# Performance work log

Measured on AMD Instinct MI355X. Metric: run time of the kernel, lower is better.

## Reference

```python
import jax, jax.numpy as jnp
import numpy as np


def _gcn(A, x, W, b):
    # GCNConv(improved=True): add_remaining_self_loops(fill=2), symmetric normalization.
    n = A.shape[0]
    idx = jnp.arange(n)
    d = jnp.diagonal(A)
    Ahat = A.at[idx, idx].set(jnp.where(d == 0, 2.0, d))  # keep existing self-loop weights
    dinv = 1.0 / jnp.sqrt(Ahat.sum(axis=1))
    return (Ahat * dinv[:, None] * dinv[None, :]) @ (x @ W) + b


def _augment(A):
    # GraphUNet.augment_adj: add self loops, A @ A (spspmm), remove self loops.
    n = A.shape[0]
    idx = jnp.arange(n)
    A1 = A.at[idx, idx].add(1.0)
    return (A1 @ A1).at[idx, idx].set(0.0)


def _pool(A, x, p, k):
    # TopKPooling with tanh nonlinearity.
    score = jnp.tanh((x @ p) / jnp.linalg.norm(p))
    vals, perm = jax.lax.top_k(score, k)
    return A[perm][:, perm], x[perm] * vals[:, None], perm


def _gat(mask, x, W, a_src, a_dst, b, heads, c, concat):
    # GATConv, eval mode (attention dropout inactive). mask[dst, src] includes self loops.
    n = x.shape[0]
    h = (x @ W).reshape(n, heads, c)
    es = jnp.einsum('shc,hc->sh', h, a_src)
    ed = jnp.einsum('dhc,hc->dh', h, a_dst)
    logits = jax.nn.leaky_relu(ed[:, None, :] + es[None, :, :], 0.2)  # [dst, src, h]
    logits = jnp.where(mask[:, :, None], logits, jnp.finfo(logits.dtype).min)
    alpha = jax.nn.softmax(logits, axis=1)  # softmax over sources per destination
    out = jnp.einsum('dsh,shc->dhc', alpha, h)
    out = out.reshape(n, heads * c) if concat else out.mean(axis=1)
    return out + b


def setup_inputs() -> dict:
    key = jax.random.key(0)
    ks = jax.random.split(key, 34)
    N, E, IN, H, OUT, HEADS = 4096, 65536, 3, 64, 128, 4
    r = lambda k, s: jax.random.normal(k, s, jnp.float32) * 0.1
    inp = {}
    inp['x'] = jax.random.normal(ks[0], (N, IN), jnp.float32)
    inp['edge_index'] = jax.random.randint(ks[1], (2, E), 0, N)
    inp['unet_w0'] = r(ks[2], (IN, H)); inp['unet_b0'] = jnp.zeros((H,), jnp.float32)
    inp['unet_w1'] = r(ks[3], (H, H)); inp['unet_b1'] = jnp.zeros((H,), jnp.float32)
    inp['unet_w2'] = r(ks[4], (H, H)); inp['unet_b2'] = jnp.zeros((H,), jnp.float32)
    inp['unet_w3'] = r(ks[5], (H, H)); inp['unet_b3'] = jnp.zeros((H,), jnp.float32)
    inp['pool_p1'] = r(ks[6], (H,)); inp['pool_p2'] = r(ks[7], (H,)); inp['pool_p3'] = r(ks[8], (H,))
    inp['up_w0'] = r(ks[9], (H, H)); inp['up_b0'] = jnp.zeros((H,), jnp.float32)
    inp['up_w1'] = r(ks[10], (H, H)); inp['up_b1'] = jnp.zeros((H,), jnp.float32)
    inp['up_w2'] = r(ks[11], (H, OUT)); inp['up_b2'] = jnp.zeros((OUT,), jnp.float32)
    inp['ln_g'] = jnp.ones((OUT,), jnp.float32); inp['ln_b'] = jnp.zeros((OUT,), jnp.float32)
    inp['res_w'] = r(ks[12], (OUT, OUT)); inp['res_b'] = jnp.zeros((OUT,), jnp.float32)
    inp['gat1_w'] = r(ks[13], (OUT, HEADS * OUT))
    inp['gat1_asrc'] = r(ks[14], (HEADS, OUT)); inp['gat1_adst'] = r(ks[15], (HEADS, OUT))
    inp['gat1_b'] = jnp.zeros((HEADS * OUT,), jnp.float32)
    inp['gat2_w'] = r(ks[16], (HEADS * OUT, OUT))
    inp['gat2_asrc'] = r(ks[17], (1, OUT)); inp['gat2_adst'] = r(ks[18], (1, OUT))
    inp['gat2_b'] = jnp.zeros((OUT,), jnp.float32)
    return inp


def reference(x, edge_index, unet_w0, unet_b0, unet_w1, unet_b1, unet_w2, unet_b2,
              unet_w3, unet_b3, pool_p1, pool_p2, pool_p3, up_w0, up_b0, up_w1, up_b1,
              up_w2, up_b2, ln_g, ln_b, res_w, res_b, gat1_w, gat1_asrc, gat1_adst,
              gat1_b, gat2_w, gat2_asrc, gat2_adst, gat2_b):
    n0 = x.shape[0]
    # Dense weighted adjacency A[dst, src]; duplicate edges accumulate weight (scatter-add).
    A0 = jnp.zeros((n0, n0), x.dtype).at[edge_index[1], edge_index[0]].add(1.0)
    # ---- GraphUNet down path ----
    x0 = jax.nn.relu(_gcn(A0, x, unet_w0, unet_b0))
    k1 = (n0 + 1) // 2
    A1, h1, perm1 = _pool(_augment(A0), x0, pool_p1, k1)
    x1 = jax.nn.relu(_gcn(A1, h1, unet_w1, unet_b1))
    k2 = (k1 + 1) // 2
    A2, h2, perm2 = _pool(_augment(A1), x1, pool_p2, k2)
    x2 = jax.nn.relu(_gcn(A2, h2, unet_w2, unet_b2))
    k3 = (k2 + 1) // 2
    A3, h3, perm3 = _pool(_augment(A2), x2, pool_p3, k3)
    x3 = jax.nn.relu(_gcn(A3, h3, unet_w3, unet_b3))
    # ---- up path (sum_res=True) ----
    h = x2 + jnp.zeros_like(x2).at[perm3].set(x3)
    h = jax.nn.relu(_gcn(A2, h, up_w0, up_b0))
    h = x1 + jnp.zeros_like(x1).at[perm2].set(h)
    h = jax.nn.relu(_gcn(A1, h, up_w1, up_b1))
    h = x0 + jnp.zeros_like(x0).at[perm1].set(h)
    h = _gcn(A0, h, up_w2, up_b2)  # last up conv: no activation -> [n0, 128]
    # ---- LayerNorm(eps=1e-6) ----
    mu = h.mean(-1, keepdims=True)
    var = ((h - mu) ** 2).mean(-1, keepdims=True)
    u = (h - mu) / jnp.sqrt(var + 1e-6) * ln_g + ln_b
    residual = u @ res_w + res_b
    mask = (A0 > 0) | jnp.eye(n0, dtype=bool)  # GATConv adds self loops
    g = jax.nn.elu(_gat(mask, u, gat1_w, gat1_asrc, gat1_adst, gat1_b, 4, 128, True))
    g = _gat(mask, g, gat2_w, gat2_asrc, gat2_adst, gat2_b, 1, 128, False)
    return g + residual
```

## Files before the change

### kernel.cpp

```cpp
#include <hip/hip_runtime.h>
#include <math.h>


#define TPB 256
#define LDK 88
#define MAXN 128

typedef __attribute__((ext_vector_type(8))) short bf16x8;
typedef __attribute__((ext_vector_type(4))) float f32x4;

__device__ inline ushort f32_to_bf16(float v) {
    unsigned b = __float_as_uint(v);
    return (ushort)((b + 0x7FFF + ((b >> 16) & 1)) >> 16);
}
__device__ inline float bf2f(ushort u) { return __uint_as_float(((unsigned)u) << 16); }

__global__ void bucket_scatter(const int* __restrict__ ei, int E, int* __restrict__ buck,
                               int* __restrict__ cursor) {
    int e = blockIdx.x * TPB + threadIdx.x;
    if (e >= E) return;
    int src = ei[e];
    int dst = ei[E + e];
    int pos = atomicAdd(&cursor[dst], 1);
    if (pos < MAXN) buck[dst * MAXN + pos] = src;
// ... 136 lines not shown
    int i = blockIdx.x;
    int o = threadIdx.x;
    __shared__ int sj[MAXN];
    __shared__ float sw_[MAXN];
    int cnt = acnt[i];
    for (int a = o; a < cnt; a += blockDim.x) {
        sj[a] = nbr[i * MAXN + a];
        sw_[a] = awt[i * MAXN + a];
    }
    __syncthreads();
    if (o >= f) return;
    float sum = 0.f;
    for (int a = 0; a < cnt; ++a) {
        int j = sj[a];
        sum += sw_[a] * (xw[(size_t)j * f + o] * dinv[j]);
    }
    float yi = xw[(size_t)i * f + o] * dinv[i];
    sum -= yi;
    float v = dinv[i] * (sum + selfw[i] * yi) + bias[o];
    if (relu) v = fmaxf(v, 0.f);
    out[(size_t)i * f + o] = v;
}

__global__ void score_kernel2(const float* __restrict__ x, const float* __restrict__ p,
                              float* __restrict__ s, int n) {
    int i = blockIdx.x * TPB + threadIdx.x;
    if (i >= n) return;
    float a = 0.f, nrm = 0.f;
    for (int c = 0; c < 64; ++c) {
        float pc = p[c];
        nrm += pc * pc;
        a += x[(size_t)i * 64 + c] * pc;
    }
    s[i] = tanhf(a / sqrtf(nrm));
}

__global__ void rank_count(const float* __restrict__ s, int n, int* __restrict__ rank) {
    __shared__ float sj[256];
    int i = blockIdx.x * 256 + threadIdx.x;
    int j0 = blockIdx.y * 256;
    sj[threadIdx.x] = s[j0 + threadIdx.x];
    float si = s[i];
    __syncthreads();
    int r = 0;
#pragma unroll 8
    for (int jj = 0; jj < 256; ++jj) {
        float v = sj[jj];
        r += (v > si) || (v == si && (j0 + jj) < i);
    }
    atomicAdd(&rank[i], r);
}

__global__ void scatter_topk_all(const float* __restrict__ s, const int* __restrict__ rank,
                                 int n, int k, int* __restrict__ perm,
                                 float* __restrict__ vals, int* __restrict__ invp) {
    int i = blockIdx.x * TPB + threadIdx.x;
    if (i >= n) return;
// ... 42 lines not shown
        dinv[r] = 1.0f / sqrtf(tot + 2.0f);
        selfw[r] = 2.0f;
    }
}

__global__ void transpose_aug_hl(const ushort* __restrict__ Ahi, const ushort* __restrict__ Alo,
                                 ushort* __restrict__ T, int n) {
    __shared__ float tile[64][65];
    int c0 = blockIdx.x * 64, r0 = blockIdx.y * 64;
    for (int t = threadIdx.x; t < 4096; t += TPB) {
        int r = t >> 6, c = t & 63;
        size_t o = (size_t)(r0 + r) * n + (c0 + c);
        float v = bf2f(Ahi[o]) + bf2f(Alo[o]);
        if (r0 + r == c0 + c) v += 1.0f;
        tile[c][r] = v;
    }
    __syncthreads();
    for (int t = threadIdx.x; t < 4096; t += TPB) {
        int c = t >> 6, r = t & 63;
        T[(size_t)(c0 + c) * n + (r0 + r)] = f32_to_bf16(tile[c][r]);
    }
}

__global__ void gather_rows_aug_hl(const ushort* __restrict__ Ahi, const ushort* __restrict__ Alo,
                                   const int* __restrict__ perm, ushort* __restrict__ Ag,
                                   int n, int rows) {
    int id = blockIdx.x * TPB + threadIdx.x;
    if (id >= rows * n) return;
    int r = id / n, t = id - r * n;
    int pr = perm[r];
    size_t o = (size_t)pr * n + t;
    float v = bf2f(Ahi[o]) + bf2f(Alo[o]);
    if (pr == t) v += 1.0f;
    Ag[id] = f32_to_bf16(v);
}

__global__ void gather_rows_u16(const ushort* __restrict__ T, const int* __restrict__ perm,
                                ushort* __restrict__ Bg, int n, int rows) {
    int id = blockIdx.x * TPB + threadIdx.x;
    if (id >= rows * n) return;
    int r = id / n, t = id - r * n;
    Bg[id] = T[(size_t)perm[r] * n + t];
}

__global__ void __launch_bounds__(256)
aug_gemm_acc(const ushort* __restrict__ Ag, const ushort* __restrict__ Bg,
             float* __restrict__ Caug, int K, int ldc, int kpb) {
    __shared__ __align__(16) ushort As[64 * LDK];
    __shared__ __align__(16) ushort Bs[64 * LDK];
    int tid = threadIdx.x;
    int wave = tid >> 6, lane = tid & 63;
    int wr = wave >> 1, wc = wave & 1;
    int m = lane & 15, quad = lane >> 4;
    int i0 = blockIdx.y * 64, j0 = blockIdx.x * 64;
    int kbeg = blockIdx.z * kpb;
    f32x4 acc[2][2];
#pragma unroll
    for (int a = 0; a < 2; ++a)
#pragma unroll
        for (int b = 0; b < 2; ++b) acc[a][b] = (f32x4){0.f, 0.f, 0.f, 0.f};
    const ushort* Ab = Ag + (size_t)i0 * K;
    const ushort* Bb = Bg + (size_t)j0 * K;
    for (int k0 = kbeg; k0 < kbeg + kpb; k0 += 64) {
#pragma unroll
        for (int v = 0; v < 2; ++v) {
// ... 119 lines not shown
#pragma unroll
        for (int ni = 0; ni < 2; ++ni)
#pragma unroll
            for (int r = 0; r < 4; ++r) {
                int gi = i0 + wr * 32 + mi * 16 + quad * 4 + r;
                int gj = j0 + wc * 32 + ni * 16 + m;
                atomicAdd(&C[(size_t)gi * ldc + gj], acc[mi][ni][r]);
            }
}

__global__ void gcn_epilogue(const float* __restrict__ C, const float* __restrict__ xw,
                             const float* __restrict__ dinv, const float* __restrict__ selfw,
                             const float* __restrict__ b, float* __restrict__ out,
                             int n, int f, int relu) {
    int id = blockIdx.x * TPB + threadIdx.x;
    if (id >= n * f) return;
    int i = id / f, c = id - i * f;
    float y = xw[id] * dinv[i];
    float v = dinv[i] * (C[id] + selfw[i] * y) + b[c];
    if (relu) v = fmaxf(v, 0.f);
    out[id] = v;
}

__global__ void layernorm(const float* __restrict__ h, const float* __restrict__ g,
                          const float* __restrict__ b, float* __restrict__ u, int n) {
    int i = blockIdx.x;
    int t = threadIdx.x;
    float v = h[(size_t)i * 128 + t];
    __shared__ float s0[2], s1[2];
    float sum = v;
    for (int o = 32; o; o >>= 1) sum += __shfl_xor(sum, o);
    if ((t & 63) == 0) s0[t >> 6] = sum;
    __syncthreads();
    float mu = (s0[0] + s0[1]) * (1.0f / 128.0f);
    float d = v - mu;
    float sq = d * d;
    for (int o = 32; o; o >>= 1) sq += __shfl_xor(sq, o);
    if ((t & 63) == 0) s1[t >> 6] = sq;
    __syncthreads();
    float var = (s1[0] + s1[1]) * (1.0f / 128.0f);
    u[(size_t)i * 128 + t] = d / sqrtf(var + 1e-6f) * g[t] + b[t];
}

__global__ void prep_weights(const float* __restrict__ rw, const float* __restrict__ g1w,
                             const float* __restrict__ g2w,
                             ushort* __restrict__ W1hi, ushort* __restrict__ W1lo,
                             ushort* __restrict__ W2hi, ushort* __restrict__ W2lo,
                             ushort* __restrict__ W3hi, ushort* __restrict__ W3lo) {
    __shared__ float tile[64][65];
    int b = blockIdx.x;
    const float* W; ushort *Bhi, *Blo; int K, Nn, bx, by;
    if (b < 4)       { W = rw;  Bhi = W1hi; Blo = W1lo; K = 128; Nn = 128; bx = b & 1;        by = b >> 1; }
    else if (b < 20) { int t = b - 4;  W = g1w; Bhi = W2hi; Blo = W2lo; K = 128; Nn = 512; bx = t & 7; by = t >> 3; }
    else             { int t = b - 20; W = g2w; Bhi = W3hi; Blo = W3lo; K = 512; Nn = 128; bx = t & 1; by = t >> 1; }
    int n0 = bx * 64, k0 = by * 64;
    for (int t = threadIdx.x; t < 4096; t += TPB) {
        int r = t >> 6, c = t & 63;
        tile[r][c] = W[(size_t)(k0 + r) * Nn + (n0 + c)];
    }
    __syncthreads();
    for (int t = threadIdx.x; t < 4096; t += TPB) {
        int c = t >> 6, r = t & 63;
        float v = tile[r][c];
        ushort hi = f32_to_bf16(v);
        size_t o = (size_t)(n0 + c) * K + (k0 + r);
        Bhi[o] = hi;
        Blo[o] = f32_to_bf16(v - bf2f(hi));
    }
}

__global__ void __launch_bounds__(256)
gemm_bt_store(const float* __restrict__ A, const ushort* __restrict__ Bhi,
              const ushort* __restrict__ Blo, const float* __restrict__ bias,
              float* __restrict__ C, int K, int N) {
    __shared__ __align__(16) ushort sAh[64 * LDK];
    __shared__ __align__(16) ushort sAl[64 * LDK];
    __shared__ __align__(16) ushort sBh[64 * LDK];
    __shared__ __align__(16) ushort sBl[64 * LDK];
    int tid = threadIdx.x;
    int wave = tid >> 6, lane = tid & 63;
    int wr = wave >> 1, wc = wave & 1;
    int m = lane & 15, quad = lane >> 4;
    int i0 = blockIdx.y * 64, j0 = blockIdx.x * 64;
    f32x4 acc[2][2];
#pragma unroll
    for (int a = 0; a < 2; ++a)
#pragma unroll
        for (int b = 0; b < 2; ++b) acc[a][b] = (f32x4){0.f, 0.f, 0.f, 0.f};
    for (int k0 = 0; k0 < K; k0 += 64) {
#pragma unroll
        for (int v = 0; v < 2; ++v) {
            int idx = tid + (v << 8);
            int r = idx >> 3, c8 = idx & 7;
            size_t boff = (size_t)(j0 + r) * K + k0 + c8 * 8;
            *(uint4*)&sBh[r * LDK + c8 * 8] = *(const uint4*)&Bhi[boff];
            *(uint4*)&sBl[r * LDK + c8 * 8] = *(const uint4*)&Blo[boff];
            size_t aoff = (size_t)(i0 + r) * K + k0 + c8 * 8;
            float4 fa = *(const float4*)&A[aoff];
            float4 fb = *(const float4*)&A[aoff + 4];
            ushort h0 = f32_to_bf16(fa.x), h1 = f32_to_bf16(fa.y);
            ushort h2 = f32_to_bf16(fa.z), h3 = f32_to_bf16(fa.w);
            ushort h4 = f32_to_bf16(fb.x), h5 = f32_to_bf16(fb.y);
            ushort h6 = f32_to_bf16(fb.z), h7 = f32_to_bf16(fb.w);
            uint4 ph, pl;
            ph.x = (uint)h0 | ((uint)h1 << 16);
            ph.y = (uint)h2 | ((uint)h3 << 16);
            ph.z = (uint)h4 | ((uint)h5 << 16);
            ph.w = (uint)h6 | ((uint)h7 << 16);
            pl.x = (uint)f32_to_bf16(fa.x - bf2f(h0)) | ((uint)f32_to_bf16(fa.y - bf2f(h1)) << 16);
            pl.y = (uint)f32_to_bf16(fa.z - bf2f(h2)) | ((uint)f32_to_bf16(fa.w - bf2f(h3)) << 16);
            pl.z = (uint)f32_to_bf16(fb.x - bf2f(h4)) | ((uint)f32_to_bf16(fb.y - bf2f(h5)) << 16);
            pl.w = (uint)f32_to_bf16(fb.z - bf2f(h6)) | ((uint)f32_to_bf16(fb.w - bf2f(h7)) << 16);
// ... 13 lines not shown
            for (int ni = 0; ni < 2; ++ni) {
                bh[ni] = *(const bf16x8*)&sBh[(wc * 32 + ni * 16 + m) * LDK + kk * 32 + quad * 8];
                bl[ni] = *(const bf16x8*)&sBl[(wc * 32 + ni * 16 + m) * LDK + kk * 32 + quad * 8];
            }
#pragma unroll
            for (int mi = 0; mi < 2; ++mi)
#pragma unroll
                for (int ni = 0; ni < 2; ++ni) {
                    acc[mi][ni] = __builtin_amdgcn_mfma_f32_16x16x32_bf16(ah[mi], bh[ni], acc[mi][ni], 0, 0, 0);
                    acc[mi][ni] = __builtin_amdgcn_mfma_f32_16x16x32_bf16(ah[mi], bl[ni], acc[mi][ni], 0, 0, 0);
                    acc[mi][ni] = __builtin_amdgcn_mfma_f32_16x16x32_bf16(al[mi], bh[ni], acc[mi][ni], 0, 0, 0);
                }
        }
        __syncthreads();
    }
#pragma unroll
    for (int mi = 0; mi < 2; ++mi)
#pragma unroll
        for (int ni = 0; ni < 2; ++ni)
#pragma unroll
            for (int r = 0; r < 4; ++r) {
                int gi = i0 + wr * 32 + mi * 16 + quad * 4 + r;
                int gj = j0 + wc * 32 + ni * 16 + m;
                float v = acc[mi][ni][r];
                if (bias) v += bias[gj];
                C[(size_t)gi * N + gj] = v;
            }
}

__global__ void __launch_bounds__(256)
gemm_bt_split(const float* __restrict__ A, const ushort* __restrict__ Bhi,
              const ushort* __restrict__ Blo, float* __restrict__ C,
              int K, int N, int kpb) {
    __shared__ __align__(16) ushort sAh[64 * LDK];
    __shared__ __align__(16) ushort sAl[64 * LDK];
    __shared__ __align__(16) ushort sBh[64 * LDK];
    __shared__ __align__(16) ushort sBl[64 * LDK];
    int tid = threadIdx.x;
    int wave = tid >> 6, lane = tid & 63;
    int wr = wave >> 1, wc = wave & 1;
    int m = lane & 15, quad = lane >> 4;
    int i0 = blockIdx.y * 64, j0 = blockIdx.x * 64;
    int kbeg = blockIdx.z * kpb;
    f32x4 acc[2][2];
#pragma unroll
    for (int a = 0; a < 2; ++a)
#pragma unroll
        for (int b = 0; b < 2; ++b) acc[a][b] = (f32x4){0.f, 0.f, 0.f, 0.f};
    for (int k0 = kbeg; k0 < kbeg + kpb; k0 += 64) {
#pragma unroll
        for (int v = 0; v < 2; ++v) {
            int idx = tid + (v << 8);
            int r = idx >> 3, c8 = idx & 7;
            size_t boff = (size_t)(j0 + r) * K + k0 + c8 * 8;
            *(uint4*)&sBh[r * LDK + c8 * 8] = *(const uint4*)&Bhi[boff];
            *(uint4*)&sBl[r * LDK + c8 * 8] = *(const uint4*)&Blo[boff];
            size_t aoff = (size_t)(i0 + r) * K + k0 + c8 * 8;
            float4 fa = *(const float4*)&A[aoff];
            float4 fb = *(const float4*)&A[aoff + 4];
            ushort h0 = f32_to_bf16(fa.x), h1 = f32_to_bf16(fa.y);
            ushort h2 = f32_to_bf16(fa.z), h3 = f32_to_bf16(fa.w);
            ushort h4 = f32_to_bf16(fb.x), h5 = f32_to_bf16(fb.y);
            ushort h6 = f32_to_bf16(fb.z), h7 = f32_to_bf16(fb.w);
            uint4 ph, pl;
            ph.x = (uint)h0 | ((uint)h1 << 16);
            ph.y = (uint)h2 | ((uint)h3 << 16);
            ph.z = (uint)h4 | ((uint)h5 << 16);
            ph.w = (uint)h6 | ((uint)h7 << 16);
            pl.x = (uint)f32_to_bf16(fa.x - bf2f(h0)) | ((uint)f32_to_bf16(fa.y - bf2f(h1)) << 16);
            pl.y = (uint)f32_to_bf16(fa.z - bf2f(h2)) | ((uint)f32_to_bf16(fa.w - bf2f(h3)) << 16);
            pl.z = (uint)f32_to_bf16(fb.x - bf2f(h4)) | ((uint)f32_to_bf16(fb.y - bf2f(h5)) << 16);
            pl.w = (uint)f32_to_bf16(fb.z - bf2f(h6)) | ((uint)f32_to_bf16(fb.w - bf2f(h7)) << 16);
            *(uint4*)&sAh[r * LDK + c8 * 8] = ph;
            *(uint4*)&sAl[r * LDK + c8 * 8] = pl;
        }
        __syncthreads();
#pragma unroll
        for (int kk = 0; kk < 2; ++kk) {
            bf16x8 ah[2], al[2], bh[2], bl[2];
#pragma unroll
            for (int mi = 0; mi < 2; ++mi) {
                ah[mi] = *(const bf16x8*)&sAh[(wr * 32 + mi * 16 + m) * LDK + kk * 32 + quad * 8];
                al[mi] = *(const bf16x8*)&sAl[(wr * 32 + mi * 16 + m) * LDK + kk * 32 + quad * 8];
            }
#pragma unroll
            for (int ni = 0; ni < 2; ++ni) {
                bh[ni] = *(const bf16x8*)&sBh[(wc * 32 + ni * 16 + m) * LDK + kk * 32 + quad * 8];
                bl[ni] = *(const bf16x8*)&sBl[(wc * 32 + ni * 16 + m) * LDK + kk * 32 + quad * 8];
            }
#pragma unroll
            for (int mi = 0; mi < 2; ++mi)
#pragma unroll
                for (int ni = 0; ni < 2; ++ni) {
                    acc[mi][ni] = __builtin_amdgcn_mfma_f32_16x16x32_bf16(ah[mi], bh[ni], acc[mi][ni], 0, 0, 0);
                    acc[mi][ni] = __builtin_amdgcn_mfma_f32_16x16x32_bf16(ah[mi], bl[ni], acc[mi][ni], 0, 0, 0);
                    acc[mi][ni] = __builtin_amdgcn_mfma_f32_16x16x32_bf16(al[mi], bh[ni], acc[mi][ni], 0, 0, 0);
                }
        }
        __syncthreads();
    }
#pragma unroll
    for (int mi = 0; mi < 2; ++mi)
#pragma unroll
        for (int ni = 0; ni < 2; ++ni)
#pragma unroll
            for (int r = 0; r < 4; ++r) {
                int gi = i0 + wr * 32 + mi * 16 + quad * 4 + r;
                int gj = j0 + wc * 32 + ni * 16 + m;
                atomicAdd(&C[(size_t)gi * N + gj], acc[mi][ni][r]);
            }
}

__global__ void attn_coef2(const float* __restrict__ hf, const float* __restrict__ asrc,
                           const float* __restrict__ adst, float* __restrict__ es,
                           float* __restrict__ ed, int heads) {
    int j = blockIdx.x;
    int wave = threadIdx.x >> 6, lane = threadIdx.x & 63;
    if (wave >= heads) return;
    const float* hp = hf + (size_t)j * heads * 128 + wave * 128;
    float v0 = hp[lane], v1 = hp[lane + 64];
    float a = v0 * asrc[wave * 128 + lane] + v1 * asrc[wave * 128 + lane + 64];
    float d = v0 * adst[wave * 128 + lane] + v1 * adst[wave * 128 + lane + 64];
    for (int o = 32; o; o >>= 1) { a += __shfl_xor(a, o); d += __shfl_xor(d, o); }
    if (lane == 0) { es[j * heads + wave] = a; ed[j * heads + wave] = d; }
}

__global__ void gat_sparse(const int* __restrict__ nbr, const int* __restrict__ ncnt, int n,
                           const float* __restrict__ hf, const float* __restrict__ es,
                           const float* __restrict__ ed, const float* __restrict__ bias,
                           const float* __restrict__ resid, float* __restrict__ out,
                           int heads, int mode) {
    int i = blockIdx.x;
    int tid = threadIdx.x;
    __shared__ int idx[MAXN];
    __shared__ float lg[MAXN * 4];
    __shared__ float hmax[4], hsum[4];
    int m = ncnt[i];
    for (int t = tid; t < m; t += TPB) idx[t] = nbr[i * MAXN + t];
    __syncthreads();
    for (int t = tid; t < m * heads; t += TPB) {
        int jl = t / heads, h = t - jl * heads;
        float l = ed[i * heads + h] + es[idx[jl] * heads + h];
        lg[jl * heads + h] = (l > 0.f) ? l : 0.2f * l;
    }
    __syncthreads();
    int h = tid >> 6, lane = tid & 63;
    if (h < heads) {
        float mx = -3.4e38f;
        for (int jl = lane; jl < m; jl += 64) mx = fmaxf(mx, lg[jl * heads + h]);
        for (int o = 32; o; o >>= 1) mx = fmaxf(mx, __shfl_xor(mx, o));
        if (lane == 0) hmax[h] = mx;
    }
    __syncthreads();
    if (h < heads) {
        float mx = hmax[h];
        float sm = 0.f;
        for (int jl = lane; jl < m; jl += 64) {
            float p = expf(lg[jl * heads + h] - mx);
            lg[jl * heads + h] = p;
            sm += p;
        }
        for (int o = 32; o; o >>= 1) sm += __shfl_xor(sm, o);
        if (lane == 0) hsum[h] = sm;
    }
    __syncthreads();
    int width = heads * 128;
    for (int o = tid; o < width; o += TPB) {
        int hh = o >> 7;
        float acc = 0.f;
        for (int jl = 0; jl < m; ++jl)
            acc += lg[jl * heads + hh] * hf[(size_t)idx[jl] * width + o];
        float v = acc / hsum[hh] + bias[o];
        if (mode == 0) v = (v > 0.f) ? v : expm1f(v);
        else v += resid[(size_t)i * width + o];
        out[(size_t)i * width + o] = v;
    }
}

static inline int cdiv(int a, int b) { return (a + b - 1) / b; }

static int pick_z(int gx, int gy, int K) {
    int z = 1;
    while (gx * gy * z < 384 && K / (2 * z) >= 64) z <<= 1;
    return z;
}

static void run_gcn_dense(hipStream_t stream, const ushort* Ahi, const ushort* Alo,
                          int n, const float* xsrc, const int* perm, const float* vals,
                          const float* hprev, const int* invp, int mode,
                          const float* W, const float* bias,
                          const float* dinv, const float* selfw,
                          float* xw, ushort* yThi, ushort* yTlo, float* Cp,
                          float* out, int relu) {
    fused_in_gemm<<<n / 4, TPB, 0, stream>>>(xsrc, perm, vals, hprev, invp, W, dinv,
                                             xw, yThi, yTlo, Cp, n, mode);
    int z = pick_z(1, n / 64, n);
    gcn_gemm<<<dim3(1, n / 64, z), TPB, 0, stream>>>(Ahi, Alo, yThi, yTlo, Cp, n, 64, n / z);
    gcn_epilogue<<<cdiv(n * 64, TPB), TPB, 0, stream>>>(Cp, xw, dinv, selfw, bias, out, n, 64, relu);
}

static void run_topk(hipStream_t stream, const float* score, int n, int k, int* rank,
                     int* perm, float* vals, int* invp) {
    hipMemsetAsync(rank, 0, n * sizeof(int), stream);
    rank_count<<<dim3(n / 256, n / 256), 256, 0, stream>>>(score, n, rank);
    scatter_topk_all<<<cdiv(n, TPB), TPB, 0, stream>>>(score, rank, n, k, perm, vals, invp);
}

static void run_aug_dense(hipStream_t stream, const ushort* Ahi, const ushort* Alo, int n,
                          const int* perm, int k, ushort* Tbf, ushort* Agb, ushort* Bgb,
                          float* Caug, ushort* Chi, ushort* Clo, float* dinv, float* selfw) {
    transpose_aug_hl<<<dim3(n / 64, n / 64), TPB, 0, stream>>>(Ahi, Alo, Tbf, n);
    gather_rows_aug_hl<<<cdiv(k * n, TPB), TPB, 0, stream>>>(Ahi, Alo, perm, Agb, n, k);
    gather_rows_u16<<<cdiv(k * n, TPB), TPB, 0, stream>>>(Tbf, perm, Bgb, n, k);
    hipMemsetAsync(Caug, 0, (size_t)k * k * sizeof(float), stream);
    int z = 8;
    aug_gemm_acc<<<dim3(k / 64, k / 64, z), TPB, 0, stream>>>(Agb, Bgb, Caug, n, k, n / z);
    aug_finalize<<<k, TPB, 0, stream>>>(Caug, k, Chi, Clo, dinv, selfw);
}

extern "C" void kernel_launch(void* const* d_in, const int* in_sizes, int n_in,
                              void* d_out, int out_size, void* d_ws, size_t ws_size,
                              hipStream_t stream) {
    const float* x   = (const float*)d_in[0];
    const int*   ei  = (const int*)d_in[1];
    const float* w0  = (const float*)d_in[2];  const float* b0  = (const float*)d_in[3];
    const float* w1  = (const float*)d_in[4];  const float* b1  = (const float*)d_in[5];
    const float* w2  = (const float*)d_in[6];  const float* b2  = (const float*)d_in[7];
    const float* w3  = (const float*)d_in[8];  const float* b3  = (const float*)d_in[9];
    const float* p1  = (const float*)d_in[10];
    const float* p2  = (const float*)d_in[11];
    const float* p3  = (const float*)d_in[12];
    const float* uw0 = (const float*)d_in[13]; const float* ub0 = (const float*)d_in[14];
    const float* uw1 = (const float*)d_in[15]; const float* ub1 = (const float*)d_in[16];
    const float* uw2 = (const float*)d_in[17]; const float* ub2 = (const float*)d_in[18];
    const float* lng = (const float*)d_in[19]; const float* lnb = (const float*)d_in[20];
    const float* rw  = (const float*)d_in[21]; const float* rb  = (const float*)d_in[22];
    const float* g1w = (const float*)d_in[23];
// ... 30 lines not shown
    float* Caug  = alloc((size_t)K2 * K2);
    float* Cp    = alloc((size_t)N * 64);
    float* x0    = alloc((size_t)N * 64);
    float* x1    = alloc((size_t)K1 * 64);
    float* x2    = alloc((size_t)K2 * 64);
    float* x3    = alloc((size_t)K3 * 64);
    float* h2    = alloc((size_t)K2 * 64);
    float* h1    = alloc((size_t)K1 * 64);
    float* xw    = alloc((size_t)N * 128);
    float* dinv0 = alloc(N);  float* selfw0 = alloc(N);
    float* dinv1 = alloc(K1); float* selfw1 = alloc(K1);
    float* dinv2 = alloc(K2); float* selfw2 = alloc(K2);
    float* dinv3 = alloc(K3); float* selfw3 = alloc(K3);
    int*   cursor= (int*)alloc(N);
    int*   buck  = (int*)alloc((size_t)N * MAXN);
    float* score = alloc(N);
    int*   rank  = (int*)alloc(N);
    float* vals1 = alloc(K1); float* vals2 = alloc(K2); float* vals3 = alloc(K3);
    int*   perm1 = (int*)alloc(K1); int* perm2 = (int*)alloc(K2); int* perm3 = (int*)alloc(K3);
    int*   invp1 = (int*)alloc(N);  int* invp2 = (int*)alloc(K1); int* invp3 = (int*)alloc(K2);
    int*   nbr   = (int*)alloc((size_t)N * MAXN);
    float* awt   = alloc((size_t)N * MAXN);
    int*   acnt  = (int*)alloc(N);
    float* hfin  = alloc((size_t)N * 128);
    float* u     = alloc((size_t)N * 128);
    float* resid = alloc((size_t)N * 128);
    float* hf1   = alloc((size_t)N * 512);
    float* es1   = alloc((size_t)N * 4); float* ed1 = alloc((size_t)N * 4);
    float* g1    = alloc((size_t)N * 512);
    float* hf2   = alloc((size_t)N * 128);
    float* es2   = alloc(N); float* ed2 = alloc(N);
    (void)ws_size; (void)n_in; (void)in_sizes; (void)out_size;

    prep_weights<<<36, TPB, 0, stream>>>(rw, g1w, g2w, W1hi, W1lo, W2hi, W2lo, W3hi, W3lo);

    hipMemsetAsync(cursor, 0, N * sizeof(int), stream);
    bucket_scatter<<<cdiv(E, TPB), TPB, 0, stream>>>(ei, E, buck, cursor);
    build_csr<<<N, 64, 0, stream>>>(buck, cursor, N, nbr, awt, acnt, dinv0, selfw0);

    xw_gemm<<<cdiv(N, TPB / 64), TPB, 0, stream>>>(x, w0, xw, N, 3, 64);
    spmv_gcn<<<N, 64, 0, stream>>>(nbr, awt, acnt, xw, dinv0, selfw0, b0, x0, 64, 1);

    score_kernel2<<<cdiv(N, TPB), TPB, 0, stream>>>(x0, p1, score, N);
    run_topk(stream, score, N, K1, rank, perm1, vals1, invp1);
    spgemm_aug<<<K1, TPB, 0, stream>>>(nbr, awt, acnt, perm1, invp1, K1,
                                       A1hi, A1lo, dinv1, selfw1);
    run_gcn_dense(stream, A1hi, A1lo, K1, x0, perm1, vals1, nullptr, nullptr, 0,
                  w1, b1, dinv1, selfw1, xw, yThi, yTlo, Cp, x1, 1);

    score_kernel2<<<cdiv(K1, TPB), TPB, 0, stream>>>(x1, p2, score, K1);
    run_topk(stream, score, K1, K2, rank, perm2, vals2, invp2);
    run_aug_dense(stream, A1hi, A1lo, K1, perm2, K2, Tbf, Agb, Bgb, Caug,
                  A2hi, A2lo, dinv2, selfw2);
    run_gcn_dense(stream, A2hi, A2lo, K2, x1, perm2, vals2, nullptr, nullptr, 0,
                  w2, b2, dinv2, selfw2, xw, yThi, yTlo, Cp, x2, 1);

    score_kernel2<<<cdiv(K2, TPB), TPB, 0, stream>>>(x2, p3, score, K2);
    run_topk(stream, score, K2, K3, rank, perm3, vals3, invp3);
    run_aug_dense(stream, A2hi, A2lo, K2, perm3, K3, Tbf, Agb, Bgb, Caug,
                  A3hi, A3lo, dinv3, selfw3);
    run_gcn_dense(stream, A3hi, A3lo, K3, x2, perm3, vals3, nullptr, nullptr, 0,
                  w3, b3, dinv3, selfw3, xw, yThi, yTlo, Cp, x3, 1);

    run_gcn_dense(stream, A2hi, A2lo, K2, x2, nullptr, nullptr, x3, invp3, 1,
                  uw0, ub0, dinv2, selfw2, xw, yThi, yTlo, Cp, h2, 1);

    run_gcn_dense(stream, A1hi, A1lo, K1, x1, nullptr, nullptr, h2, invp2, 1,
                  uw1, ub1, dinv1, selfw1, xw, yThi, yTlo, Cp, h1, 1);

    xw_gemm_unpool<<<N / 2, TPB, 0, stream>>>(x0, h1, invp1, uw2, xw, N);
    spmv_gcn<<<N, 128, 0, stream>>>(nbr, awt, acnt, xw, dinv0, selfw0, ub2, hfin, 128, 0);

    layernorm<<<N, 128, 0, stream>>>(hfin, lng, lnb, u, N);
    gemm_bt_store<<<dim3(2, N / 64), TPB, 0, stream>>>(u, W1hi, W1lo, rb, resid, 128, 128);

    gemm_bt_store<<<dim3(8, N / 64), TPB, 0, stream>>>(u, W2hi, W2lo, nullptr, hf1, 128, 512);
    attn_coef2<<<N, 256, 0, stream>>>(hf1, g1as, g1ad, es1, ed1, 4);
    gat_sparse<<<N, TPB, 0, stream>>>(nbr, acnt, N, hf1, es1, ed1, g1b, nullptr, g1, 4, 0);

    hipMemsetAsync(hf2, 0, (size_t)N * 128 * sizeof(float), stream);
    gemm_bt_split<<<dim3(2, N / 64, 4), TPB, 0, stream>>>(g1, W3hi, W3lo, hf2, 512, 128, 128);
    attn_coef2<<<N, 64, 0, stream>>>(hf2, g2as, g2ad, es2, ed2, 1);
    gat_sparse<<<N, TPB, 0, stream>>>(nbr, acnt, N, hf2, es2, ed2, g2b, resid, (float*)d_out, 1, 1);
}
```

Measured before the change: 457.6 us.

## Fuse tail kernels, fold memsets, and store GAT features in bf16

Fuses the final GCN spmv with LayerNorm and merges the residual and GAT1 projection GEMMs into one launch. The GAT1 hidden features are now stored as bf16, and the GAT kernels are split into specialized 4-head and 1-head versions. Several memsets are folded into existing kernels (rank zeroing, Caug zeroing, hf2 zeroing), and the two row-gather kernels become a single launch. The aim is to cut launch count and memory traffic, at the cost of some precision in the GAT1 features.

```diff
diff --git a/kernel.cpp b/kernel.cpp
--- a/kernel.cpp
+++ b/kernel.cpp
@@ -182,8 +182,46 @@
     out[(size_t)i * f + o] = v;
 }
 
+__global__ void spmv_gcn_ln(const int* __restrict__ nbr, const float* __restrict__ awt,
+                            const int* __restrict__ acnt, const float* __restrict__ xw,
+                            const float* __restrict__ dinv, const float* __restrict__ selfw,
+                            const float* __restrict__ bias, const float* __restrict__ g,
+                            const float* __restrict__ lb, float* __restrict__ u) {
+    int i = blockIdx.x;
+    int o = threadIdx.x;
+    __shared__ int sj[MAXN];
+    __shared__ float sw_[MAXN];
+    __shared__ float s0[2], s1[2];
+    int cnt = acnt[i];
+    for (int a = o; a < cnt; a += 128) {
+        sj[a] = nbr[i * MAXN + a];
+        sw_[a] = awt[i * MAXN + a];
+    }
+    __syncthreads();
+    float sum = 0.f;
+    for (int a = 0; a < cnt; ++a) {
+        int j = sj[a];
+        sum += sw_[a] * (xw[(size_t)j * 128 + o] * dinv[j]);
+    }
+    float yi = xw[(size_t)i * 128 + o] * dinv[i];
+    sum -= yi;
+    float v = dinv[i] * (sum + selfw[i] * yi) + bias[o];
+    float s = v;
+    for (int off = 32; off; off >>= 1) s += __shfl_xor(s, off);
+    if ((o & 63) == 0) s0[o >> 6] = s;
+    __syncthreads();
+    float mu = (s0[0] + s0[1]) * (1.0f / 128.0f);
+    float d = v - mu;
+    float sq = d * d;
+    for (int off = 32; off; off >>= 1) sq += __shfl_xor(sq, off);
+    if ((o & 63) == 0) s1[o >> 6] = sq;
+    __syncthreads();
+    float var = (s1[0] + s1[1]) * (1.0f / 128.0f);
+    u[(size_t)i * 128 + o] = d / sqrtf(var + 1e-6f) * g[o] + lb[o];
+}
+
 __global__ void score_kernel2(const float* __restrict__ x, const float* __restrict__ p,
-                              float* __restrict__ s, int n) {
+                              float* __restrict__ s, int* __restrict__ rank, int n) {
     int i = blockIdx.x * TPB + threadIdx.x;
     if (i >= n) return;
     float a = 0.f, nrm = 0.f;
@@ -193,6 +231,7 @@
         a += x[(size_t)i * 64 + c] * pc;
     }
     s[i] = tanhf(a / sqrtf(nrm));
+    rank[i] = 0;
 }
 
 __global__ void rank_count(const float* __restrict__ s, int n, int* __restrict__ rank) {
@@ -281,25 +320,23 @@
     }
 }
 
-__global__ void gather_rows_aug_hl(const ushort* __restrict__ Ahi, const ushort* __restrict__ Alo,
-                                   const int* __restrict__ perm, ushort* __restrict__ Ag,
-                                   int n, int rows) {
+__global__ void gather_both(const ushort* __restrict__ Ahi, const ushort* __restrict__ Alo,
+                            const ushort* __restrict__ T, const int* __restrict__ perm,
+                            ushort* __restrict__ Ag, ushort* __restrict__ Bg,
+                            float* __restrict__ Caug, int n, int k) {
     int id = blockIdx.x * TPB + threadIdx.x;
-    if (id >= rows * n) return;
+    if (id >= k * n) return;
     int r = id / n, t = id - r * n;
-    int pr = perm[r];
-    size_t o = (size_t)pr * n + t;
-    float v = bf2f(Ahi[o]) + bf2f(Alo[o]);
-    if (pr == t) v += 1.0f;
-    Ag[id] = f32_to_bf16(v);
-}
-
-__global__ void gather_rows_u16(const ushort* __restrict__ T, const int* __restrict__ perm,
-                                ushort* __restrict__ Bg, int n, int rows) {
-    int id = blockIdx.x * TPB + threadIdx.x;
-    if (id >= rows * n) return;
-    int r = id / n, t = id - r * n;
-    Bg[id] = T[(size_t)perm[r] * n + t];
+    if (blockIdx.y == 0) {
+        int pr = perm[r];
+        size_t o = (size_t)pr * n + t;
+        float v = bf2f(Ahi[o]) + bf2f(Alo[o]);
+        if (pr == t) v += 1.0f;
+        Ag[id] = f32_to_bf16(v);
+        if (t < k) Caug[(size_t)r * k + t] = 0.f;
+    } else {
+        Bg[id] = T[(size_t)perm[r] * n + t];
+    }
 }
 
 __global__ void __launch_bounds__(256)
@@ -465,26 +502,6 @@
     out[id] = v;
 }
 
-__global__ void layernorm(const float* __restrict__ h, const float* __restrict__ g,
-                          const float* __restrict__ b, float* __restrict__ u, int n) {
-    int i = blockIdx.x;
-    int t = threadIdx.x;
-    float v = h[(size_t)i * 128 + t];
-    __shared__ float s0[2], s1[2];
-    float sum = v;
-    for (int o = 32; o; o >>= 1) sum += __shfl_xor(sum, o);
-    if ((t & 63) == 0) s0[t >> 6] = sum;
-    __syncthreads();
-    float mu = (s0[0] + s0[1]) * (1.0f / 128.0f);
-    float d = v - mu;
-    float sq = d * d;
-    for (int o = 32; o; o >>= 1) sq += __shfl_xor(sq, o);
-    if ((t & 63) == 0) s1[t >> 6] = sq;
-    __syncthreads();
-    float var = (s1[0] + s1[1]) * (1.0f / 128.0f);
-    u[(size_t)i * 128 + t] = d / sqrtf(var + 1e-6f) * g[t] + b[t];
-}
-
 __global__ void prep_weights(const float* __restrict__ rw, const float* __restrict__ g1w,
                              const float* __restrict__ g2w,
                              ushort* __restrict__ W1hi, ushort* __restrict__ W1lo,
@@ -513,9 +530,99 @@
 }
 
 __global__ void __launch_bounds__(256)
-gemm_bt_store(const float* __restrict__ A, const ushort* __restrict__ Bhi,
-              const ushort* __restrict__ Blo, const float* __restrict__ bias,
-              float* __restrict__ C, int K, int N) {
+gemm_bt_multi(const float* __restrict__ A,
+              const ushort* __restrict__ W1hi, const ushort* __restrict__ W1lo,
+              const float* __restrict__ rb, float* __restrict__ resid,
+              const ushort* __restrict__ W2hi, const ushort* __restrict__ W2lo,
+              ushort* __restrict__ hf1b) {
+    __shared__ __align__(16) ushort sAh[64 * LDK];
+    __shared__ __align__(16) ushort sAl[64 * LDK];
+    __shared__ __align__(16) ushort sBh[64 * LDK];
+    __shared__ __align__(16) ushort sBl[64 * LDK];
+    int tid = threadIdx.x;
+    int wave = tid >> 6, lane = tid & 63;
+    int wr = wave >> 1, wc = wave & 1;
+    int m = lane & 15, quad = lane >> 4;
+    int b = blockIdx.x;
+    const ushort *Bhi, *Blo; int j0; bool tohf;
+    if (b < 2) { Bhi = W1hi; Blo = W1lo; j0 = b * 64; tohf = false; }
+    else       { Bhi = W2hi; Blo = W2lo; j0 = (b - 2) * 64; tohf = true; }
+    int i0 = blockIdx.y * 64;
+    f32x4 acc[2][2];
+#pragma unroll
+    for (int a = 0; a < 2; ++a)
+#pragma unroll
+        for (int bb = 0; bb < 2; ++bb) acc[a][bb] = (f32x4){0.f, 0.f, 0.f, 0.f};
+    for (int k0 = 0; k0 < 128; k0 += 64) {
+#pragma unroll
+        for (int v = 0; v < 2; ++v) {
+            int idx = tid + (v << 8);
+            int r = idx >> 3, c8 = idx & 7;
+            size_t boff = (size_t)(j0 + r) * 128 + k0 + c8 * 8;
+            *(uint4*)&sBh[r * LDK + c8 * 8] = *(const uint4*)&Bhi[boff];
+            *(uint4*)&sBl[r * LDK + c8 * 8] = *(const uint4*)&Blo[boff];
+            size_t aoff = (size_t)(i0 + r) * 128 + k0 + c8 * 8;
+            float4 fa = *(const float4*)&A[aoff];
+            float4 fb = *(const float4*)&A[aoff + 4];
+            ushort h0 = f32_to_bf16(fa.x), h1 = f32_to_bf16(fa.y);
+            ushort h2 = f32_to_bf16(fa.z), h3 = f32_to_bf16(fa.w);
+            ushort h4 = f32_to_bf16(fb.x), h5 = f32_to_bf16(fb.y);
+            ushort h6 = f32_to_bf16(fb.z), h7 = f32_to_bf16(fb.w);
+            uint4 ph, pl;
+            ph.x = (uint)h0 | ((uint)h1 << 16);
+            ph.y = (uint)h2 | ((uint)h3 << 16);
+            ph.z = (uint)h4 | ((uint)h5 << 16);
+            ph.w = (uint)h6 | ((uint)h7 << 16);
+            pl.x = (uint)f32_to_bf16(fa.x - bf2f(h0)) | ((uint)f32_to_bf16(fa.y - bf2f(h1)) << 16);
+            pl.y = (uint)f32_to_bf16(fa.z - bf2f(h2)) | ((uint)f32_to_bf16(fa.w - bf2f(h3)) << 16);
+            pl.z = (uint)f32_to_bf16(fb.x - bf2f(h4)) | ((uint)f32_to_bf16(fb.y - bf2f(h5)) << 16);
+            pl.w = (uint)f32_to_bf16(fb.z - bf2f(h6)) | ((uint)f32_to_bf16(fb.w - bf2f(h7)) << 16);
+            *(uint4*)&sAh[r * LDK + c8 * 8] = ph;
+            *(uint4*)&sAl[r * LDK + c8 * 8] = pl;
+        }
+        __syncthreads();
+#pragma unroll
+        for (int kk = 0; kk < 2; ++kk) {
+            bf16x8 ah[2], al[2], bh[2], bl[2];
+#pragma unroll
+            for (int mi = 0; mi < 2; ++mi) {
+                ah[mi] = *(const bf16x8*)&sAh[(wr * 32 + mi * 16 + m) * LDK + kk * 32 + quad * 8];
+                al[mi] = *(const bf16x8*)&sAl[(wr * 32 + mi * 16 + m) * LDK + kk * 32 + quad * 8];
+            }
+#pragma unroll
+            for (int ni = 0; ni < 2; ++ni) {
+                bh[ni] = *(const bf16x8*)&sBh[(wc * 32 + ni * 16 + m) * LDK + kk * 32 + quad * 8];
+                bl[ni] = *(const bf16x8*)&sBl[(wc * 32 + ni * 16 + m) * LDK + kk * 32 + quad * 8];
+            }
+#pragma unroll
+            for (int mi = 0; mi < 2; ++mi)
+#pragma unroll
+                for (int ni = 0; ni < 2; ++ni) {
+                    acc[mi][ni] = __builtin_amdgcn_mfma_f32_16x16x32_bf16(ah[mi], bh[ni], acc[mi][ni], 0, 0, 0);
+                    acc[mi][ni] = __builtin_amdgcn_mfma_f32_16x16x32_bf16(ah[mi], bl[ni], acc[mi][ni], 0, 0, 0);
+                    acc[mi][ni] = __builtin_amdgcn_mfma_f32_16x16x32_bf16(al[mi], bh[ni], acc[mi][ni], 0, 0, 0);
+                }
+        }
+        __syncthreads();
+    }
+#pragma unroll
+    for (int mi = 0; mi < 2; ++mi)
+#pragma unroll
+        for (int ni = 0; ni < 2; ++ni)
+#pragma unroll
+            for (int r = 0; r < 4; ++r) {
+                int gi = i0 + wr * 32 + mi * 16 + quad * 4 + r;
+                int gj = j0 + wc * 32 + ni * 16 + m;
+                float v = acc[mi][ni][r];
+                if (tohf) hf1b[(size_t)gi * 512 + gj] = f32_to_bf16(v);
+                else      resid[(size_t)gi * 128 + gj] = v + rb[gj];
+            }
+}
+
+__global__ void __launch_bounds__(256)
+gemm_bt_split(const float* __restrict__ A, const ushort* __restrict__ Bhi,
+              const ushort* __restrict__ Blo, float* __restrict__ C,
+              int K, int N, int kpb) {
     __shared__ __align__(16) ushort sAh[64 * LDK];
     __shared__ __align__(16) ushort sAl[64 * LDK];
     __shared__ __align__(16) ushort sBh[64 * LDK];
@@ -525,12 +632,13 @@
     int wr = wave >> 1, wc = wave & 1;
     int m = lane & 15, quad = lane >> 4;
     int i0 = blockIdx.y * 64, j0 = blockIdx.x * 64;
+    int kbeg = blockIdx.z * kpb;
     f32x4 acc[2][2];
 #pragma unroll
     for (int a = 0; a < 2; ++a)
 #pragma unroll
         for (int b = 0; b < 2; ++b) acc[a][b] = (f32x4){0.f, 0.f, 0.f, 0.f};
-    for (int k0 = 0; k0 < K; k0 += 64) {
+    for (int k0 = kbeg; k0 < kbeg + kpb; k0 += 64) {
 #pragma unroll
         for (int v = 0; v < 2; ++v) {
             int idx = tid + (v << 8);
@@ -590,93 +698,22 @@
             for (int r = 0; r < 4; ++r) {
                 int gi = i0 + wr * 32 + mi * 16 + quad * 4 + r;
                 int gj = j0 + wc * 32 + ni * 16 + m;
-                float v = acc[mi][ni][r];
-                if (bias) v += bias[gj];
-                C[(size_t)gi * N + gj] = v;
-            }
-}
-
-__global__ void __launch_bounds__(256)
-gemm_bt_split(const float* __restrict__ A, const ushort* __restrict__ Bhi,
-              const ushort* __restrict__ Blo, float* __restrict__ C,
-              int K, int N, int kpb) {
-    __shared__ __align__(16) ushort sAh[64 * LDK];
-    __shared__ __align__(16) ushort sAl[64 * LDK];
-    __shared__ __align__(16) ushort sBh[64 * LDK];
-    __shared__ __align__(16) ushort sBl[64 * LDK];
-    int tid = threadIdx.x;
-    int wave = tid >> 6, lane = tid & 63;
-    int wr = wave >> 1, wc = wave & 1;
-    int m = lane & 15, quad = lane >> 4;
-    int i0 = blockIdx.y * 64, j0 = blockIdx.x * 64;
-    int kbeg = blockIdx.z * kpb;
-    f32x4 acc[2][2];
-#pragma unroll
-    for (int a = 0; a < 2; ++a)
-#pragma unroll
-        for (int b = 0; b < 2; ++b) acc[a][b] = (f32x4){0.f, 0.f, 0.f, 0.f};
-    for (int k0 = kbeg; k0 < kbeg + kpb; k0 += 64) {
-#pragma unroll
-        for (int v = 0; v < 2; ++v) {
-            int idx = tid + (v << 8);
-            int r = idx >> 3, c8 = idx & 7;
-            size_t boff = (size_t)(j0 + r) * K + k0 + c8 * 8;
-            *(uint4*)&sBh[r * LDK + c8 * 8] = *(const uint4*)&Bhi[boff];
-            *(uint4*)&sBl[r * LDK + c8 * 8] = *(const uint4*)&Blo[boff];
-            size_t aoff = (size_t)(i0 + r) * K + k0 + c8 * 8;
-            float4 fa = *(const float4*)&A[aoff];
-            float4 fb = *(const float4*)&A[aoff + 4];
-            ushort h0 = f32_to_bf16(fa.x), h1 = f32_to_bf16(fa.y);
-            ushort h2 = f32_to_bf16(fa.z), h3 = f32_to_bf16(fa.w);
-            ushort h4 = f32_to_bf16(fb.x), h5 = f32_to_bf16(fb.y);
-            ushort h6 = f32_to_bf16(fb.z), h7 = f32_to_bf16(fb.w);
-            uint4 ph, pl;
-            ph.x = (uint)h0 | ((uint)h1 << 16);
-            ph.y = (uint)h2 | ((uint)h3 << 16);
-            ph.z = (uint)h4 | ((uint)h5 << 16);
-            ph.w = (uint)h6 | ((uint)h7 << 16);
-            pl.x = (uint)f32_to_bf16(fa.x - bf2f(h0)) | ((uint)f32_to_bf16(fa.y - bf2f(h1)) << 16);
-            pl.y = (uint)f32_to_bf16(fa.z - bf2f(h2)) | ((uint)f32_to_bf16(fa.w - bf2f(h3)) << 16);
-            pl.z = (uint)f32_to_bf16(fb.x - bf2f(h4)) | ((uint)f32_to_bf16(fb.y - bf2f(h5)) << 16);
-            pl.w = (uint)f32_to_bf16(fb.z - bf2f(h6)) | ((uint)f32_to_bf16(fb.w - bf2f(h7)) << 16);
-            *(uint4*)&sAh[r * LDK + c8 * 8] = ph;
-            *(uint4*)&sAl[r * LDK + c8 * 8] = pl;
-        }
-        __syncthreads();
-#pragma unroll
-        for (int kk = 0; kk < 2; ++kk) {
-            bf16x8 ah[2], al[2], bh[2], bl[2];
-#pragma unroll
-            for (int mi = 0; mi < 2; ++mi) {
-                ah[mi] = *(const bf16x8*)&sAh[(wr * 32 + mi * 16 + m) * LDK + kk * 32 + quad * 8];
-                al[mi] = *(const bf16x8*)&sAl[(wr * 32 + mi * 16 + m) * LDK + kk * 32 + quad * 8];
-            }
-#pragma unroll
-            for (int ni = 0; ni < 2; ++ni) {
-                bh[ni] = *(const bf16x8*)&sBh[(wc * 32 + ni * 16 + m) * LDK + kk * 32 + quad * 8];
-                bl[ni] = *(const bf16x8*)&sBl[(wc * 32 + ni * 16 + m) * LDK + kk * 32 + quad * 8];
-            }
-#pragma unroll
-            for (int mi = 0; mi < 2; ++mi)
-#pragma unroll
-                for (int ni = 0; ni < 2; ++ni) {
-                    acc[mi][ni] = __builtin_amdgcn_mfma_f32_16x16x32_bf16(ah[mi], bh[ni], acc[mi][ni], 0, 0, 0);
-                    acc[mi][ni] = __builtin_amdgcn_mfma_f32_16x16x32_bf16(ah[mi], bl[ni], acc[mi][ni], 0, 0, 0);
-                    acc[mi][ni] = __builtin_amdgcn_mfma_f32_16x16x32_bf16(al[mi], bh[ni], acc[mi][ni], 0, 0, 0);
-                }
-        }
-        __syncthreads();
-    }
-#pragma unroll
-    for (int mi = 0; mi < 2; ++mi)
-#pragma unroll
-        for (int ni = 0; ni < 2; ++ni)
-#pragma unroll
-            for (int r = 0; r < 4; ++r) {
-                int gi = i0 + wr * 32 + mi * 16 + quad * 4 + r;
-                int gj = j0 + wc * 32 + ni * 16 + m;
                 atomicAdd(&C[(size_t)gi * N + gj], acc[mi][ni][r]);
             }
+}
+
+__global__ void attn_coef2_b16(const ushort* __restrict__ hf, const float* __restrict__ asrc,
+                               const float* __restrict__ adst, float* __restrict__ es,
+                               float* __restrict__ ed, int heads) {
+    int j = blockIdx.x;
+    int wave = threadIdx.x >> 6, lane = threadIdx.x & 63;
+    if (wave >= heads) return;
+    const ushort* hp = hf + (size_t)j * heads * 128 + wave * 128;
+    float v0 = bf2f(hp[lane]), v1 = bf2f(hp[lane + 64]);
+    float a = v0 * asrc[wave * 128 + lane] + v1 * asrc[wave * 128 + lane + 64];
+    float d = v0 * adst[wave * 128 + lane] + v1 * adst[wave * 128 + lane + 64];
+    for (int o = 32; o; o >>= 1) { a += __shfl_xor(a, o); d += __shfl_xor(d, o); }
+    if (lane == 0) { es[j * heads + wave] = a; ed[j * heads + wave] = d; }
 }
 
 __global__ void attn_coef2(const float* __restrict__ hf, const float* __restrict__ asrc,
@@ -693,16 +730,17 @@
     if (lane == 0) { es[j * heads + wave] = a; ed[j * heads + wave] = d; }
 }
 
-__global__ void gat_sparse(const int* __restrict__ nbr, const int* __restrict__ ncnt, int n,
-                           const float* __restrict__ hf, const float* __restrict__ es,
-                           const float* __restrict__ ed, const float* __restrict__ bias,
-                           const float* __restrict__ resid, float* __restrict__ out,
-                           int heads, int mode) {
+__global__ void gat_sparse_b16(const int* __restrict__ nbr, const int* __restrict__ ncnt, int n,
+                               const ushort* __restrict__ hf, const float* __restrict__ es,
+                               const float* __restrict__ ed, const float* __restrict__ bias,
+                               float* __restrict__ out, float* __restrict__ zbuf) {
+    const int heads = 4;
     int i = blockIdx.x;
     int tid = threadIdx.x;
     __shared__ int idx[MAXN];
     __shared__ float lg[MAXN * 4];
     __shared__ float hmax[4], hsum[4];
+    for (int o2 = tid; o2 < 128; o2 += TPB) zbuf[(size_t)i * 128 + o2] = 0.f;
     int m = ncnt[i];
     for (int t = tid; t < m; t += TPB) idx[t] = nbr[i * MAXN + t];
     __syncthreads();
@@ -713,14 +751,14 @@
     }
     __syncthreads();
     int h = tid >> 6, lane = tid & 63;
-    if (h < heads) {
+    {
         float mx = -3.4e38f;
         for (int jl = lane; jl < m; jl += 64) mx = fmaxf(mx, lg[jl * heads + h]);
         for (int o = 32; o; o >>= 1) mx = fmaxf(mx, __shfl_xor(mx, o));
         if (lane == 0) hmax[h] = mx;
     }
     __syncthreads();
-    if (h < heads) {
+    {
         float mx = hmax[h];
         float sm = 0.f;
         for (int jl = lane; jl < m; jl += 64) {
@@ -732,16 +770,59 @@
         if (lane == 0) hsum[h] = sm;
     }
     __syncthreads();
-    int width = heads * 128;
-    for (int o = tid; o < width; o += TPB) {
+    for (int o = tid; o < 512; o += TPB) {
         int hh = o >> 7;
         float acc = 0.f;
         for (int jl = 0; jl < m; ++jl)
-            acc += lg[jl * heads + hh] * hf[(size_t)idx[jl] * width + o];
+            acc += lg[jl * heads + hh] * bf2f(hf[(size_t)idx[jl] * 512 + o]);
         float v = acc / hsum[hh] + bias[o];
-        if (mode == 0) v = (v > 0.f) ? v : expm1f(v);
-        else v += resid[(size_t)i * width + o];
-        out[(size_t)i * width + o] = v;
+        v = (v > 0.f) ? v : expm1f(v);
+        out[(size_t)i * 512 + o] = v;
+    }
+}
+
+__global__ void gat_sparse(const int* __restrict__ nbr, const int* __restrict__ ncnt, int n,
+                           const float* __restrict__ hf, const float* __restrict__ es,
+                           const float* __restrict__ ed, const float* __restrict__ bias,
+                           const float* __restrict__ resid, float* __restrict__ out) {
+    int i = blockIdx.x;
+    int tid = threadIdx.x;
+    __shared__ int idx[MAXN];
+    __shared__ float lg[MAXN];
+    __shared__ float hmax1, hsum1;
+    int m = ncnt[i];
+    for (int t = tid; t < m; t += TPB) idx[t] = nbr[i * MAXN + t];
+    __syncthreads();
+    for (int t = tid; t < m; t += TPB) {
+        float l = ed[i] + es[idx[t]];
+        lg[t] = (l > 0.f) ? l : 0.2f * l;
+    }
+    __syncthreads();
+    int lane = tid & 63;
+    if (tid < 64) {
+        float mx = -3.4e38f;
+        for (int jl = lane; jl < m; jl += 64) mx = fmaxf(mx, lg[jl]);
+        for (int o = 32; o; o >>= 1) mx = fmaxf(mx, __shfl_xor(mx, o));
+        if (lane == 0) hmax1 = mx;
+    }
+    __syncthreads();
+    if (tid < 64) {
+        float mx = hmax1;
+        float sm = 0.f;
+        for (int jl = lane; jl < m; jl += 64) {
+            float p = expf(lg[jl] - mx);
+            lg[jl] = p;
+            sm += p;
+        }
+        for (int o = 32; o; o >>= 1) sm += __shfl_xor(sm, o);
+        if (lane == 0) hsum1 = sm;
+    }
+    __syncthreads();
+    for (int o = tid; o < 128; o += TPB) {
+        float acc = 0.f;
+        for (int jl = 0; jl < m; ++jl)
+            acc += lg[jl] * hf[(size_t)idx[jl] * 128 + o];
+        out[(size_t)i * 128 + o] = acc / hsum1 + bias[o] + resid[(size_t)i * 128 + o];
     }
 }
 
@@ -769,7 +850,6 @@
 
 static void run_topk(hipStream_t stream, const float* score, int n, int k, int* rank,
                      int* perm, float* vals, int* invp) {
-    hipMemsetAsync(rank, 0, n * sizeof(int), stream);
     rank_count<<<dim3(n / 256, n / 256), 256, 0, stream>>>(score, n, rank);
     scatter_topk_all<<<cdiv(n, TPB), TPB, 0, stream>>>(score, rank, n, k, perm, vals, invp);
 }
@@ -778,9 +858,8 @@
                           const int* perm, int k, ushort* Tbf, ushort* Agb, ushort* Bgb,
                           float* Caug, ushort* Chi, ushort* Clo, float* dinv, float* selfw) {
     transpose_aug_hl<<<dim3(n / 64, n / 64), TPB, 0, stream>>>(Ahi, Alo, Tbf, n);
-    gather_rows_aug_hl<<<cdiv(k * n, TPB), TPB, 0, stream>>>(Ahi, Alo, perm, Agb, n, k);
-    gather_rows_u16<<<cdiv(k * n, TPB), TPB, 0, stream>>>(Tbf, perm, Bgb, n, k);
-    hipMemsetAsync(Caug, 0, (size_t)k * k * sizeof(float), stream);
+    gather_both<<<dim3(cdiv(k * n, TPB), 2), TPB, 0, stream>>>(Ahi, Alo, Tbf, perm,
+                                                               Agb, Bgb, Caug, n, k);
     int z = 8;
     aug_gemm_acc<<<dim3(k / 64, k / 64, z), TPB, 0, stream>>>(Agb, Bgb, Caug, n, k, n / z);
     aug_finalize<<<k, TPB, 0, stream>>>(Caug, k, Chi, Clo, dinv, selfw);
@@ -857,10 +936,9 @@
     int*   nbr   = (int*)alloc((size_t)N * MAXN);
     float* awt   = alloc((size_t)N * MAXN);
     int*   acnt  = (int*)alloc(N);
-    float* hfin  = alloc((size_t)N * 128);
     float* u     = alloc((size_t)N * 128);
     float* resid = alloc((size_t)N * 128);
-    float* hf1   = alloc((size_t)N * 512);
+    ushort* hf1b = (ushort*)alloc((size_t)N * 512 / 2);
     float* es1   = alloc((size_t)N * 4); float* ed1 = alloc((size_t)N * 4);
     float* g1    = alloc((size_t)N * 512);
     float* hf2   = alloc((size_t)N * 128);
@@ -876,21 +954,21 @@
     xw_gemm<<<cdiv(N, TPB / 64), TPB, 0, stream>>>(x, w0, xw, N, 3, 64);
     spmv_gcn<<<N, 64, 0, stream>>>(nbr, awt, acnt, xw, dinv0, selfw0, b0, x0, 64, 1);
 
-    score_kernel2<<<cdiv(N, TPB), TPB, 0, stream>>>(x0, p1, score, N);
+    score_kernel2<<<cdiv(N, TPB), TPB, 0, stream>>>(x0, p1, score, rank, N);
     run_topk(stream, score, N, K1, rank, perm1, vals1, invp1);
     spgemm_aug<<<K1, TPB, 0, stream>>>(nbr, awt, acnt, perm1, invp1, K1,
                                        A1hi, A1lo, dinv1, selfw1);
     run_gcn_dense(stream, A1hi, A1lo, K1, x0, perm1, vals1, nullptr, nullptr, 0,
                   w1, b1, dinv1, selfw1, xw, yThi, yTlo, Cp, x1, 1);
 
-    score_kernel2<<<cdiv(K1, TPB), TPB, 0, stream>>>(x1, p2, score, K1);
+    score_kernel2<<<cdiv(K1, TPB), TPB, 0, stream>>>(x1, p2, score, rank, K1);
     run_topk(stream, score, K1, K2, rank, perm2, vals2, invp2);
     run_aug_dense(stream, A1hi, A1lo, K1, perm2, K2, Tbf, Agb, Bgb, Caug,
                   A2hi, A2lo, dinv2, selfw2);
     run_gcn_dense(stream, A2hi, A2lo, K2, x1, perm2, vals2, nullptr, nullptr, 0,
                   w2, b2, dinv2, selfw2, xw, yThi, yTlo, Cp, x2, 1);
 
-    score_kernel2<<<cdiv(K2, TPB), TPB, 0, stream>>>(x2, p3, score, K2);
+    score_kernel2<<<cdiv(K2, TPB), TPB, 0, stream>>>(x2, p3, score, rank, K2);
     run_topk(stream, score, K2, K3, rank, perm3, vals3, invp3);
     run_aug_dense(stream, A2hi, A2lo, K2, perm3, K3, Tbf, Agb, Bgb, Caug,
                   A3hi, A3lo, dinv3, selfw3);
@@ -904,17 +982,15 @@
                   uw1, ub1, dinv1, selfw1, xw, yThi, yTlo, Cp, h1, 1);
 
     xw_gemm_unpool<<<N / 2, TPB, 0, stream>>>(x0, h1, invp1, uw2, xw, N);
-    spmv_gcn<<<N, 128, 0, stream>>>(nbr, awt, acnt, xw, dinv0, selfw0, ub2, hfin, 128, 0);
-
-    layernorm<<<N, 128, 0, stream>>>(hfin, lng, lnb, u, N);
-    gemm_bt_store<<<dim3(2, N / 64), TPB, 0, stream>>>(u, W1hi, W1lo, rb, resid, 128, 128);
-
-    gemm_bt_store<<<dim3(8, N / 64), TPB, 0, stream>>>(u, W2hi, W2lo, nullptr, hf1, 128, 512);
-    attn_coef2<<<N, 256, 0, stream>>>(hf1, g1as, g1ad, es1, ed1, 4);
-    gat_sparse<<<N, TPB, 0, stream>>>(nbr, acnt, N, hf1, es1, ed1, g1b, nullptr, g1, 4, 0);
-
-    hipMemsetAsync(hf2, 0, (size_t)N * 128 * sizeof(float), stream);
+    spmv_gcn_ln<<<N, 128, 0, stream>>>(nbr, awt, acnt, xw, dinv0, selfw0, ub2, lng, lnb, u);
+
+    gemm_bt_multi<<<dim3(10, N / 64), TPB, 0, stream>>>(u, W1hi, W1lo, rb, resid,
+                                                        W2hi, W2lo, hf1b);
+
+    attn_coef2_b16<<<N, 256, 0, stream>>>(hf1b, g1as, g1ad, es1, ed1, 4);
+    gat_sparse_b16<<<N, TPB, 0, stream>>>(nbr, acnt, N, hf1b, es1, ed1, g1b, g1, hf2);
+
     gemm_bt_split<<<dim3(2, N / 64, 4), TPB, 0, stream>>>(g1, W3hi, W3lo, hf2, 512, 128, 128);
     attn_coef2<<<N, 64, 0, stream>>>(hf2, g2as, g2ad, es2, ed2, 1);
-    gat_sparse<<<N, TPB, 0, stream>>>(nbr, acnt, N, hf2, es2, ed2, g2b, resid, (float*)d_out, 1, 1);
-}
+    gat_sparse<<<N, TPB, 0, stream>>>(nbr, acnt, N, hf2, es2, ed2, g2b, resid, (float*)d_out);
+}
```

After: 438.6 us. 1.04x faster.
